# Optimization experiments

Hardware: AMD Instinct MI355X
Metric: run time of the kernel (lower is better)

## Reference

```python
import jax, jax.numpy as jnp
import numpy as np

B, S, D, H = 32, 512, 512, 8
DH = D // H
EXP_FF, EXP_CONV, K = 4, 2, 31
EPS = 1e-5


def _layernorm(x, g, b):
    m = jnp.mean(x, axis=-1, keepdims=True)
    v = jnp.mean(jnp.square(x - m), axis=-1, keepdims=True)
    return (x - m) * jax.lax.rsqrt(v + EPS) * g + b


def _sinusoid_pe(s, d):
    pos = np.arange(s, dtype=np.float32)[:, None]
    i = np.arange(0, d, 2, dtype=np.float32)[None, :]
    ang = pos / np.power(10000.0, i / d)
    pe = np.zeros((s, d), dtype=np.float32)
    pe[:, 0::2] = np.sin(ang)
    pe[:, 1::2] = np.cos(ang)
    return jnp.asarray(pe)


def _rel_shift(ps):
    # Transformer-XL relative shift on [b,h,s,s]
    b, h, s1, s2 = ps.shape
    p = jnp.pad(ps, ((0, 0), (0, 0), (0, 0), (1, 0)))
    p = p.reshape(b, h, s2 + 1, s1)
    return p[:, :, 1:].reshape(b, h, s1, s2)


def setup_inputs() -> dict:
    key = jax.random.key(0)
    ks = iter(jax.random.split(key, 64))
    nrm = lambda shape, sc=0.02: jax.random.normal(next(ks), shape, jnp.float32) * sc
    ones = lambda n: jnp.ones((n,), jnp.float32)
    zeros = lambda n: jnp.zeros((n,), jnp.float32)
    return {
        'x': jax.random.normal(next(ks), (B, S, D), jnp.float32),
        'ff1_g': ones(D), 'ff1_b': zeros(D),
        'ff1_w1': nrm((D, EXP_FF * D)), 'ff1_b1': zeros(EXP_FF * D),
        'ff1_w2': nrm((EXP_FF * D, D)), 'ff1_b2': zeros(D),
        'attn_g': ones(D), 'attn_b': zeros(D),
        'wq': nrm((D, D)), 'bq': zeros(D),
        'wk': nrm((D, D)), 'bk': zeros(D),
        'wv': nrm((D, D)), 'bv': zeros(D),
        'wpos': nrm((D, D)),
        'u_bias': nrm((H, DH)), 'v_bias': nrm((H, DH)),
        'wo': nrm((D, D)), 'bo': zeros(D),
        'conv_g': ones(D), 'conv_b': zeros(D),
        'pw1_w': nrm((D, EXP_CONV * D)), 'pw1_b': zeros(EXP_CONV * D),
        'dw_w': nrm((D, 1, K)),
        'bn_g': ones(D), 'bn_b': zeros(D), 'bn_m': zeros(D), 'bn_v': ones(D),
        'pw2_w': nrm((D, D)), 'pw2_b': zeros(D),
        'ff2_g': ones(D), 'ff2_b': zeros(D),
        'ff2_w1': nrm((D, EXP_FF * D)), 'ff2_b1': zeros(EXP_FF * D),
        'ff2_w2': nrm((EXP_FF * D, D)), 'ff2_b2': zeros(D),
        'ln_g': ones(D), 'ln_b': zeros(D),
    }


def _ff(x, g, b, w1, b1, w2, b2):
    y = _layernorm(x, g, b)
    return jnp.dot(jax.nn.silu(jnp.dot(y, w1) + b1), w2) + b2


def reference(x, ff1_g, ff1_b, ff1_w1, ff1_b1, ff1_w2, ff1_b2,
              attn_g, attn_b, wq, bq, wk, bk, wv, bv, wpos, u_bias, v_bias, wo, bo,
              conv_g, conv_b, pw1_w, pw1_b, dw_w, bn_g, bn_b, bn_m, bn_v, pw2_w, pw2_b,
              ff2_g, ff2_b, ff2_w1, ff2_b1, ff2_w2, ff2_b2, ln_g, ln_b):
    b, s, d = x.shape
    # Macaron FF 1 (half-step residual)
    out = x + 0.5 * _ff(x, ff1_g, ff1_b, ff1_w1, ff1_b1, ff1_w2, ff1_b2)
    # Relative-position multi-head self-attention
    y = _layernorm(out, attn_g, attn_b)
    pe = _sinusoid_pe(s, d)
    q = (jnp.dot(y, wq) + bq).reshape(b, s, H, DH)
    k = (jnp.dot(y, wk) + bk).reshape(b, s, H, DH)
    v = (jnp.dot(y, wv) + bv).reshape(b, s, H, DH)
    p = jnp.dot(pe, wpos).reshape(s, H, DH)
    content = jnp.einsum('bqhd,bkhd->bhqk', q + u_bias, k)
    pos = _rel_shift(jnp.einsum('bqhd,khd->bhqk', q + v_bias, p))
    attn = jax.nn.softmax((content + pos) / np.sqrt(d).astype(np.float32), axis=-1)
    ctx = jnp.einsum('bhqk,bkhd->bqhd', attn, v).reshape(b, s, d)
    out = out + (jnp.dot(ctx, wo) + bo)
    y = _layernorm(out, conv_g, conv_b)
    y = jnp.dot(y, pw1_w) + pw1_b                     # [b,s,2d]
    a, gate = jnp.split(y, 2, axis=-1)
    y = (a * jax.nn.sigmoid(gate)).transpose(0, 2, 1)  # [b,d,s]
    pad = (K - 1) // 2
    y = jax.lax.conv_general_dilated(y, dw_w, (1,), [(pad, pad)],
                                     dimension_numbers=('NCH', 'OIH', 'NCH'),
                                     feature_group_count=d)
    y = (y - bn_m[None, :, None]) * jax.lax.rsqrt(bn_v + EPS)[None, :, None] \
        * bn_g[None, :, None] + bn_b[None, :, None]
    y = jax.nn.silu(y).transpose(0, 2, 1)             # [b,s,d]
    out = out + (jnp.dot(y, pw2_w) + pw2_b)
    # Macaron FF 2 + final LN
    out = out + 0.5 * _ff(out, ff2_g, ff2_b, ff2_w1, ff2_b1, ff2_w2, ff2_b2)
    out = _layernorm(out, ln_g, ln_b)
    return out, attn
```

## Files before the change

### kernel.cpp

```cpp
#include <hip/hip_runtime.h>
#include <cstddef>
#include <cstdint>

#define EPSF 1e-5f

constexpr int BB = 32, SS = 512, DD = 512, HH = 8, DH = 64;
constexpr int NTOK = BB * SS;
constexpr size_t ND = (size_t)NTOK * DD;

typedef __attribute__((ext_vector_type(8))) short bf16x8;
typedef __attribute__((ext_vector_type(4))) float f32x4;

__device__ __forceinline__ float sigmf(float v) { return 1.f / (1.f + __expf(-v)); }

__device__ __forceinline__ ushort f2bf(float f) {
  union { float f; uint32_t u; } x{f};
  uint32_t r = x.u + 0x7FFF + ((x.u >> 16) & 1);
  return (ushort)(r >> 16);
}
__device__ __forceinline__ float bf2f(ushort u) {
  union { uint32_t u; float f; } x{(uint32_t)u << 16};
  return x.f;
}

__device__ __forceinline__ void gload16(const ushort* g, ushort* ldsbase) {
  __builtin_amdgcn_global_load_lds((const __attribute__((address_space(1))) void*)g,
                                   (__attribute__((address_space(3))) void*)ldsbase, 16, 0, 0);
}

__device__ __forceinline__ void xcd_swz(int& bx, int& by) {
  const int gx = gridDim.x;
  const int nwg = gx * gridDim.y;
  const int cpx = nwg >> 3;
  int id = by * gx + bx;
  id = (id & 7) * cpx + (id >> 3);
  bx = id % gx;
  by = id / gx;
}

__global__ __launch_bounds__(256) void ln_f32(const float* __restrict__ x,
                                              const float* __restrict__ g,
                                              const float* __restrict__ b,
                                              float* __restrict__ y) {
  const int lane = threadIdx.x & 63;
  const int row = blockIdx.x * 4 + (threadIdx.x >> 6);
  const float* xr = x + (size_t)row * 512;
  const float4 v0 = *(const float4*)&xr[lane << 2];
  const float4 v1 = *(const float4*)&xr[256 + (lane << 2)];
  float s = v0.x + v0.y + v0.z + v0.w + v1.x + v1.y + v1.z + v1.w;
#pragma unroll
  for (int o = 32; o > 0; o >>= 1) s += __shfl_xor(s, o);
  const float mean = s * (1.f / 512.f);
  float q = 0.f;
  q += (v0.x - mean) * (v0.x - mean); q += (v0.y - mean) * (v0.y - mean);
  q += (v0.z - mean) * (v0.z - mean); q += (v0.w - mean) * (v0.w - mean);
  q += (v1.x - mean) * (v1.x - mean); q += (v1.y - mean) * (v1.y - mean);
  q += (v1.z - mean) * (v1.z - mean); q += (v1.w - mean) * (v1.w - mean);
#pragma unroll
  for (int o = 32; o > 0; o >>= 1) q += __shfl_xor(q, o);
  const float rs = rsqrtf(q * (1.f / 512.f) + EPSF);
  const float4 g0 = *(const float4*)&g[lane << 2];
  const float4 g1 = *(const float4*)&g[256 + (lane << 2)];
  const float4 b0 = *(const float4*)&b[lane << 2];
  const float4 b1 = *(const float4*)&b[256 + (lane << 2)];
  float* yr = y + (size_t)row * 512;
  float4 o0, o1;
  o0.x = (v0.x - mean) * rs * g0.x + b0.x; o0.y = (v0.y - mean) * rs * g0.y + b0.y;
  o0.z = (v0.z - mean) * rs * g0.z + b0.z; o0.w = (v0.w - mean) * rs * g0.w + b0.w;
  o1.x = (v1.x - mean) * rs * g1.x + b1.x; o1.y = (v1.y - mean) * rs * g1.y + b1.y;
  o1.z = (v1.z - mean) * rs * g1.z + b1.z; o1.w = (v1.w - mean) * rs * g1.w + b1.w;
  *(float4*)&yr[lane << 2] = o0;
  *(float4*)&yr[256 + (lane << 2)] = o1;
}

__global__ __launch_bounds__(256) void ln_bf16(const float* __restrict__ x,
                                               const float* __restrict__ g,
                                               const float* __restrict__ b,
                                               ushort* __restrict__ y) {
  const int lane = threadIdx.x & 63;
  const int row = blockIdx.x * 4 + (threadIdx.x >> 6);
  const float* xr = x + (size_t)row * 512;
  const float4 v0 = *(const float4*)&xr[lane << 2];
  const float4 v1 = *(const float4*)&xr[256 + (lane << 2)];
  float s = v0.x + v0.y + v0.z + v0.w + v1.x + v1.y + v1.z + v1.w;
#pragma unroll
  for (int o = 32; o > 0; o >>= 1) s += __shfl_xor(s, o);
  const float mean = s * (1.f / 512.f);
  float q = 0.f;
  q += (v0.x - mean) * (v0.x - mean); q += (v0.y - mean) * (v0.y - mean);
  q += (v0.z - mean) * (v0.z - mean); q += (v0.w - mean) * (v0.w - mean);
  q += (v1.x - mean) * (v1.x - mean); q += (v1.y - mean) * (v1.y - mean);
  q += (v1.z - mean) * (v1.z - mean); q += (v1.w - mean) * (v1.w - mean);
#pragma unroll
  for (int o = 32; o > 0; o >>= 1) q += __shfl_xor(q, o);
  const float rs = rsqrtf(q * (1.f / 512.f) + EPSF);
  const float4 g0 = *(const float4*)&g[lane << 2];
  const float4 g1 = *(const float4*)&g[256 + (lane << 2)];
  const float4 b0 = *(const float4*)&b[lane << 2];
  const float4 b1 = *(const float4*)&b[256 + (lane << 2)];
  ushort* yr = y + (size_t)row * 512;
  ushort4 o0, o1;
  o0.x = f2bf((v0.x - mean) * rs * g0.x + b0.x); o0.y = f2bf((v0.y - mean) * rs * g0.y + b0.y);
  o0.z = f2bf((v0.z - mean) * rs * g0.z + b0.z); o0.w = f2bf((v0.w - mean) * rs * g0.w + b0.w);
  o1.x = f2bf((v1.x - mean) * rs * g1.x + b1.x); o1.y = f2bf((v1.y - mean) * rs * g1.y + b1.y);
  o1.z = f2bf((v1.z - mean) * rs * g1.z + b1.z); o1.w = f2bf((v1.w - mean) * rs * g1.w + b1.w);
  *(ushort4*)&yr[lane << 2] = o0;
  *(ushort4*)&yr[256 + (lane << 2)] = o1;
}

struct TpArgs {
  const float* src[11];
  ushort* dst[11];
  int K[11];
  int N[11];
  int base[12];
};

__global__ __launch_bounds__(256) void transpose_all(TpArgs a) {
  __shared__ float tile[32][33];
  int s = 0;
  const int bid = blockIdx.x;
  while (s < 10 && bid >= a.base[s + 1]) ++s;
  const int r = bid - a.base[s];
  const int K = a.K[s], N = a.N[s];
  const int ntx = N >> 5;
  const int n0 = (r % ntx) << 5;
  const int k0 = (r / ntx) << 5;
  const float* in = a.src[s];
  ushort* out = a.dst[s];
  const int tx = threadIdx.x & 31, ty = threadIdx.x >> 5;
#pragma unroll
  for (int i = 0; i < 32; i += 8)
    tile[ty + i][tx] = in[(size_t)(k0 + ty + i) * N + n0 + tx];
  __syncthreads();
#pragma unroll
  for (int i = 0; i < 32; i += 8)
    out[(size_t)(n0 + ty + i) * K + k0 + tx] = f2bf(tile[tx][ty + i]);
}

template <int ACT, int RES, int HB, int OBF>
__global__ __launch_bounds__(256) void gemm_bf16(const ushort* __restrict__ A,
                                                 const ushort* __restrict__ Wt,
                                                 const float* __restrict__ bias,
                                                 const float* __restrict__ res,
                                                 void* __restrict__ Cv,
                                                 int M, int K, int N) {
  __shared__ ushort Al[2][8192];
  __shared__ ushort Bl[2][8192];
  const int t = threadIdx.x;
  const int lane = t & 63;
  const int w = t >> 6;
  const int wr = (w >> 1) << 6, wc = (w & 1) << 6;
  int bx = blockIdx.x, by = blockIdx.y;
  xcd_swz(bx, by);
  const int m0 = by << 7, n0 = bx << 7;
  const int lm = lane & 15;
  const int grow = lane >> 3;
  const int gcol = (lane & 7) << 3;

  f32x4 acc[4][4];
#pragma unroll
  for (int i = 0; i < 4; ++i)
#pragma unroll
    for (int j = 0; j < 4; ++j) acc[i][j] = (f32x4)(0.f);

  const int NT = K >> 6;
#pragma unroll
  for (int i = 0; i < 4; ++i) {
    const int s = (w << 2) + i;
    gload16(A + (size_t)(m0 + (s << 3) + grow) * K + gcol, &Al[0][s << 9]);
    gload16(Wt + (size_t)(n0 + (s << 3) + grow) * K + gcol, &Bl[0][s << 9]);
  }
  __syncthreads();
  int cur = 0;
  for (int tt = 0; tt < NT; ++tt) {
    if (tt + 1 < NT) {
      const int k0 = (tt + 1) << 6;
#pragma unroll
      for (int i = 0; i < 4; ++i) {
        const int s = (w << 2) + i;
        gload16(A + (size_t)(m0 + (s << 3) + grow) * K + k0 + gcol, &Al[cur ^ 1][s << 9]);
        gload16(Wt + (size_t)(n0 + (s << 3) + grow) * K + k0 + gcol, &Bl[cur ^ 1][s << 9]);
      }
    }
#pragma unroll
    for (int ks = 0; ks < 2; ++ks) {
      const int kof = (ks << 5) + ((lane >> 4) << 3);
      bf16x8 af[4], bfr[4];
#pragma unroll
      for (int i = 0; i < 4; ++i) af[i] = *(const bf16x8*)&Al[cur][(wr + (i << 4) + lm) * 64 + kof];
#pragma unroll
      for (int j = 0; j < 4; ++j) bfr[j] = *(const bf16x8*)&Bl[cur][(wc + (j << 4) + lm) * 64 + kof];
#pragma unroll
      for (int i = 0; i < 4; ++i)
#pragma unroll
        for (int j = 0; j < 4; ++j)
          acc[i][j] = __builtin_amdgcn_mfma_f32_16x16x32_bf16(af[i], bfr[j], acc[i][j], 0, 0, 0);
    }
    __syncthreads();
    cur ^= 1;
  }

  float bb[4] = {0.f, 0.f, 0.f, 0.f};
  if (HB) {
#pragma unroll
    for (int j = 0; j < 4; ++j) bb[j] = bias[n0 + wc + j * 16 + lm];
  }
  const int rbase = m0 + wr + ((lane >> 4) << 2);
#pragma unroll
  for (int i = 0; i < 4; ++i) {
#pragma unroll
    for (int r = 0; r < 4; ++r) {
      const size_t row = (size_t)(rbase + i * 16 + r);
#pragma unroll
      for (int j = 0; j < 4; ++j) {
        const int col = n0 + wc + j * 16 + lm;
        float v = acc[i][j][r] + bb[j];
        if (ACT == 1) v = v * sigmf(v);
        if (RES == 1) v += res[row * N + col];
        else if (RES == 2) v = res[row * N + col] + 0.5f * v;
        if (OBF) ((ushort*)Cv)[row * N + col] = f2bf(v);
        else ((float*)Cv)[row * N + col] = v;
      }
    }
  }
}

__global__ __launch_bounds__(256) void gemm_qkv(const ushort* __restrict__ A,
                                                const ushort* __restrict__ Wt,
                                                const float* __restrict__ bq,
                                                const float* __restrict__ bk,
                                                const float* __restrict__ bv,
                                                const float* __restrict__ ub,
                                                const float* __restrict__ vb,
                                                ushort* __restrict__ qu,
                                                ushort* __restrict__ qv,
                                                ushort* __restrict__ kbb,
                                                ushort* __restrict__ vT,
                                                int M, int K) {
  __shared__ ushort Al[2][8192];
  __shared__ ushort Bl[2][8192];
  const int t = threadIdx.x;
  const int lane = t & 63;
  const int w = t >> 6;
  const int wr = (w >> 1) << 6, wc = (w & 1) << 6;
  int bx = blockIdx.x, by = blockIdx.y;
  xcd_swz(bx, by);
  const int m0 = by << 7, n0 = bx << 7;
  const int lm = lane & 15;
  const int grow = lane >> 3;
  const int gcol = (lane & 7) << 3;
  f32x4 acc[4][4];
#pragma unroll
  for (int i = 0; i < 4; ++i)
#pragma unroll
    for (int j = 0; j < 4; ++j) acc[i][j] = (f32x4)(0.f);
  const int NT = K >> 6;
#pragma unroll
  for (int i = 0; i < 4; ++i) {
    const int s = (w << 2) + i;
    gload16(A + (size_t)(m0 + (s << 3) + grow) * K + gcol, &Al[0][s << 9]);
    gload16(Wt + (size_t)(n0 + (s << 3) + grow) * K + gcol, &Bl[0][s << 9]);
  }
  __syncthreads();
  int cur = 0;
  for (int tt = 0; tt < NT; ++tt) {
    if (tt + 1 < NT) {
      const int k0 = (tt + 1) << 6;
#pragma unroll
      for (int i = 0; i < 4; ++i) {
        const int s = (w << 2) + i;
        gload16(A + (size_t)(m0 + (s << 3) + grow) * K + k0 + gcol, &Al[cur ^ 1][s << 9]);
        gload16(Wt + (size_t)(n0 + (s << 3) + grow) * K + k0 + gcol, &Bl[cur ^ 1][s << 9]);
      }
    }
#pragma unroll
    for (int ks = 0; ks < 2; ++ks) {
      const int kof = (ks << 5) + ((lane >> 4) << 3);
      bf16x8 af[4], bfr[4];
#pragma unroll
      for (int i = 0; i < 4; ++i) af[i] = *(const bf16x8*)&Al[cur][(wr + (i << 4) + lm) * 64 + kof];
#pragma unroll
      for (int j = 0; j < 4; ++j) bfr[j] = *(const bf16x8*)&Bl[cur][(wc + (j << 4) + lm) * 64 + kof];
#pragma unroll
      for (int i = 0; i < 4; ++i)
#pragma unroll
        for (int j = 0; j < 4; ++j)
          acc[i][j] = __builtin_amdgcn_mfma_f32_16x16x32_bf16(af[i], bfr[j], acc[i][j], 0, 0, 0);
    }
    __syncthreads();
    cur ^= 1;
  }
  const int seg = n0 >> 9;
  const int nloc = n0 & 511;
  const float* bsel = (seg == 0) ? bq : (seg == 1 ? bk : bv);
  float bb[4], uu[4], vv[4];
#pragma unroll
  for (int j = 0; j < 4; ++j) {
    const int col = nloc + wc + j * 16 + lm;
    bb[j] = bsel[col];
    if (seg == 0) { uu[j] = ub[col]; vv[j] = vb[col]; }
  }
  const int rbase = m0 + wr + ((lane >> 4) << 2);
  if (seg == 2) {
    const int bloc = m0 >> 9;
    const int sbase = rbase - (bloc << 9);
#pragma unroll
    for (int i = 0; i < 4; ++i) {
#pragma unroll
      for (int j = 0; j < 4; ++j) {
        const int col = nloc + wc + j * 16 + lm;
        ushort4 o;
        o.x = f2bf(acc[i][j][0] + bb[j]);
        o.y = f2bf(acc[i][j][1] + bb[j]);
        o.z = f2bf(acc[i][j][2] + bb[j]);
        o.w = f2bf(acc[i][j][3] + bb[j]);
        *(ushort4*)&vT[((size_t)((bloc << 9) + col)) * 512 + sbase + i * 16] = o;
      }
    }
    return;
  }
#pragma unroll
  for (int i = 0; i < 4; ++i) {
#pragma unroll
    for (int r = 0; r < 4; ++r) {
      const size_t row = (size_t)(rbase + i * 16 + r);
#pragma unroll
      for (int j = 0; j < 4; ++j) {
        const int col = nloc + wc + j * 16 + lm;
        const float v = acc[i][j][r] + bb[j];
        if (seg == 0) {
          qu[row * 512 + col] = f2bf(v + uu[j]);
          qv[row * 512 + col] = f2bf(v + vv[j]);
        } else {
          kbb[row * 512 + col] = f2bf(v);
        }
      }
    }
  }
}

__global__ __launch_bounds__(256) void gemm_glu(const ushort* __restrict__ A,
                                                const ushort* __restrict__ Wt,
                                                const float* __restrict__ bias,
                                                ushort* __restrict__ Cout,
                                                int M, int K) {
  __shared__ ushort Al[8192];
  __shared__ ushort Ba[8192];
  __shared__ ushort Bg[8192];
  const int t = threadIdx.x;
  const int lane = t & 63;
  const int w = t >> 6;
  const int wr = (w >> 1) << 6, wc = (w & 1) << 6;
  int bx = blockIdx.x, by = blockIdx.y;
  xcd_swz(bx, by);
  const int m0 = by << 7, n0 = bx << 7;
  const int lm = lane & 15;
  const int grow = lane >> 3;
  const int gcol = (lane & 7) << 3;
  const ushort* WtA = Wt;
  const ushort* WtG = Wt + (size_t)512 * 512;
  f32x4 acca[4][4], accg[4][4];
#pragma unroll
  for (int i = 0; i < 4; ++i)
#pragma unroll
    for (int j = 0; j < 4; ++j) { acca[i][j] = (f32x4)(0.f); accg[i][j] = (f32x4)(0.f); }
  const int NT = K >> 6;
  for (int tt = 0; tt < NT; ++tt) {
    const int k0 = tt << 6;
    if (tt) __syncthreads();
#pragma unroll
    for (int i = 0; i < 4; ++i) {
      const int s = (w << 2) + i;
      gload16(A + (size_t)(m0 + (s << 3) + grow) * K + k0 + gcol, &Al[s << 9]);
      gload16(WtA + (size_t)(n0 + (s << 3) + grow) * K + k0 + gcol, &Ba[s << 9]);
      gload16(WtG + (size_t)(n0 + (s << 3) + grow) * K + k0 + gcol, &Bg[s << 9]);
    }
    __syncthreads();
#pragma unroll
    for (int ks = 0; ks < 2; ++ks) {
      const int kof = (ks << 5) + ((lane >> 4) << 3);
      bf16x8 af[4], ba4[4], bg4[4];
#pragma unroll
      for (int i = 0; i < 4; ++i) af[i] = *(const bf16x8*)&Al[(wr + (i << 4) + lm) * 64 + kof];
#pragma unroll
      for (int j = 0; j < 4; ++j) {
        ba4[j] = *(const bf16x8*)&Ba[(wc + (j << 4) + lm) * 64 + kof];
        bg4[j] = *(const bf16x8*)&Bg[(wc + (j << 4) + lm) * 64 + kof];
      }
#pragma unroll
      for (int i = 0; i < 4; ++i)
#pragma unroll
        for (int j = 0; j < 4; ++j) {
          acca[i][j] = __builtin_amdgcn_mfma_f32_16x16x32_bf16(af[i], ba4[j], acca[i][j], 0, 0, 0);
          accg[i][j] = __builtin_amdgcn_mfma_f32_16x16x32_bf16(af[i], bg4[j], accg[i][j], 0, 0, 0);
        }
    }
  }
  float bba[4], bbg[4];
#pragma unroll
  for (int j = 0; j < 4; ++j) {
    const int col = n0 + wc + j * 16 + lm;
    bba[j] = bias[col];
    bbg[j] = bias[512 + col];
  }
  const int rbase = m0 + wr + ((lane >> 4) << 2);
#pragma unroll
  for (int i = 0; i < 4; ++i) {
#pragma unroll
    for (int r = 0; r < 4; ++r) {
      const size_t row = (size_t)(rbase + i * 16 + r);
#pragma unroll
      for (int j = 0; j < 4; ++j) {
        const int col = n0 + wc + j * 16 + lm;
        const float va = acca[i][j][r] + bba[j];
        const float vg = accg[i][j][r] + bbg[j];
        Cout[row * 512 + col] = f2bf(va * sigmf(vg));
      }
    }
  }
}

__global__ void pe_kernel_bf16(ushort* __restrict__ pe) {
  const int pos = blockIdx.x, ii = threadIdx.x;
  const float ang = (float)pos * powf(10000.f, -(float)(2 * ii) / 512.f);
  pe[((size_t)pos << 9) + 2 * ii] = f2bf(sinf(ang));
  pe[((size_t)pos << 9) + 2 * ii + 1] = f2bf(cosf(ang));
}

__global__ __launch_bounds__(256) void attn_fused3(const ushort* __restrict__ qu,
                                                   const ushort* __restrict__ qv,
                                                   const ushort* __restrict__ kbb,
                                                   const ushort* __restrict__ ppb,
                                                   const ushort* __restrict__ vT,
                                                   float* __restrict__ attn,
                                                   ushort* __restrict__ ctx) {
  __shared__ ushort psL[65][520];
  __shared__ ushort stage[64][72];
  const int t = threadIdx.x, lane = t & 63, w = t >> 6;
  const int z = blockIdx.y, b = z >> 3, h = z & 7;
  const int q0 = blockIdx.x << 6;
  const int lm = lane & 15, lk = (lane >> 4) << 3;
  const int fr4 = (lane >> 4) << 2;
  const int srow = t >> 2, scol = (t & 3) << 4;

  const size_t qoff = ((size_t)((b << 9) + q0 + (w << 4) + lm)) * 512 + (h << 6);
  bf16x8 a0 = *(const bf16x8*)&qv[qoff + lk];
  bf16x8 a1 = *(const bf16x8*)&qv[qoff + lk + 32];
  int er = q0 + 64 + lm;
  if (er > 511) er = 511;
  const size_t eoff = ((size_t)((b << 9) + er)) * 512 + (h << 6);
  const bf16x8 e0 = *(const bf16x8*)&qv[eoff + lk];
  const bf16x8 e1 = *(const bf16x8*)&qv[eoff + lk + 32];
  const ushort* pb_ = ppb + (h << 6);
#pragma unroll
  for (int tile = 0; tile < 8; ++tile) {
    __syncthreads();
    {
      const ushort* src = &pb_[(size_t)((tile << 6) + srow) * 512 + scol];
      *(bf16x8*)&stage[srow][scol] = *(const bf16x8*)src;
      *(bf16x8*)&stage[srow][scol + 8] = *(const bf16x8*)(src + 8);
    }
    __syncthreads();
#pragma unroll
    for (int ctl = 0; ctl < 4; ++ctl) {
      const bf16x8 b0 = *(const bf16x8*)&stage[(ctl << 4) + lm][lk];
      const bf16x8 b1 = *(const bf16x8*)&stage[(ctl << 4) + lm][lk + 32];
      f32x4 a = (f32x4)(0.f);
      a = __builtin_amdgcn_mfma_f32_16x16x32_bf16(a0, b0, a, 0, 0, 0);
      a = __builtin_amdgcn_mfma_f32_16x16x32_bf16(a1, b1, a, 0, 0, 0);
      const int col = (tile << 6) + (ctl << 4) + lm;
#pragma unroll
      for (int r = 0; r < 4; ++r) psL[(w << 4) + fr4 + r][col] = f2bf(a[r]);
    }
    {
      const bf16x8 b0 = *(const bf16x8*)&stage[(w << 4) + lm][lk];
      const bf16x8 b1 = *(const bf16x8*)&stage[(w << 4) + lm][lk + 32];
      f32x4 a = (f32x4)(0.f);
      a = __builtin_amdgcn_mfma_f32_16x16x32_bf16(e0, b0, a, 0, 0, 0);
      a = __builtin_amdgcn_mfma_f32_16x16x32_bf16(e1, b1, a, 0, 0, 0);
      if ((lane >> 4) == 0) psL[64][(tile << 6) + (w << 4) + lm] = f2bf(a[0]);
    }
  }

  a0 = *(const bf16x8*)&qu[qoff + lk];
  a1 = *(const bf16x8*)&qu[qoff + lk + 32];
  const ushort* kb_ = kbb + ((size_t)(b << 9)) * 512 + (h << 6);
  f32x4 acc[32];
#pragma unroll
  for (int i = 0; i < 32; ++i) acc[i] = (f32x4)(0.f);
#pragma unroll
  for (int tile = 0; tile < 8; ++tile) {
    __syncthreads();
    {
      const ushort* src = &kb_[(size_t)((tile << 6) + srow) * 512 + scol];
      *(bf16x8*)&stage[srow][scol] = *(const bf16x8*)src;
      *(bf16x8*)&stage[srow][scol + 8] = *(const bf16x8*)(src + 8);
    }
    __syncthreads();
#pragma unroll
    for (int ctl = 0; ctl < 4; ++ctl) {
      const int ct = (tile << 2) + ctl;
      const bf16x8 b0 = *(const bf16x8*)&stage[(ctl << 4) + lm][lk];
      const bf16x8 b1 = *(const bf16x8*)&stage[(ctl << 4) + lm][lk + 32];
      acc[ct] = __builtin_amdgcn_mfma_f32_16x16x32_bf16(a0, b0, acc[ct], 0, 0, 0);
      acc[ct] = __builtin_amdgcn_mfma_f32_16x16x32_bf16(a1, b1, acc[ct], 0, 0, 0);
    }
  }

  const float scale = 0.044194173824159216f;
  const int qb_ = q0 + (w << 4) + fr4;
#pragma unroll
  for (int ct = 0; ct < 32; ++ct) {
#pragma unroll
    for (int r = 0; r < 4; ++r) {
      const int q = qb_ + r;
      const int qq = q - q0;
      const int c = (ct << 4) + lm;
      float f;
      if (c <= q)          f = bf2f(psL[qq][c - q + 511]);
      else if (c == q + 1) f = 0.f;
      else                 f = bf2f(psL[qq + 1][c - q - 2]);
      acc[ct][r] = (acc[ct][r] + f) * scale;
    }
  }
  float mx[4] = {-3.0e38f, -3.0e38f, -3.0e38f, -3.0e38f};
#pragma unroll
  for (int ct = 0; ct < 32; ++ct)
#pragma unroll
    for (int r = 0; r < 4; ++r) mx[r] = fmaxf(mx[r], acc[ct][r]);
#pragma unroll
  for (int o = 1; o < 16; o <<= 1)
#pragma unroll
    for (int r = 0; r < 4; ++r) mx[r] = fmaxf(mx[r], __shfl_xor(mx[r], o));
  float sme[4] = {0.f, 0.f, 0.f, 0.f};
#pragma unroll
  for (int ct = 0; ct < 32; ++ct)
#pragma unroll
    for (int r = 0; r < 4; ++r) {
      acc[ct][r] = __expf(acc[ct][r] - mx[r]);
      sme[r] += acc[ct][r];
    }
#pragma unroll
  for (int o = 1; o < 16; o <<= 1)
#pragma unroll
    for (int r = 0; r < 4; ++r) sme[r] += __shfl_xor(sme[r], o);
#pragma unroll
  for (int r = 0; r < 4; ++r) {
    const float inv = 1.f / sme[r];
#pragma unroll
    for (int ct = 0; ct < 32; ++ct) acc[ct][r] *= inv;
  }
  float* arow = attn + ((size_t)((b << 3) + h) << 18);
#pragma unroll
  for (int ct = 0; ct < 32; ++ct)
#pragma unroll
    for (int r = 0; r < 4; ++r)
      arow[(size_t)(qb_ + r) * 512 + (ct << 4) + lm] = acc[ct][r];
  ushort* Pl = &psL[0][0];
  f32x4 acc2[4];
#pragma unroll
  for (int i = 0; i < 4; ++i) acc2[i] = (f32x4)(0.f);
  const ushort* vtb = vT + ((size_t)((b << 9) + (h << 6))) * 512;
#pragma unroll
  for (int ch = 0; ch < 8; ++ch) {
    __syncthreads();
#pragma unroll
    for (int ctl = 0; ctl < 4; ++ctl) {
      const int ct = (ch << 2) + ctl;
#pragma unroll
      for (int r = 0; r < 4; ++r)
        Pl[((w << 4) + fr4 + r) * 72 + (ctl << 4) + lm] = f2bf(acc[ct][r]);
    }
    {
      const ushort* src = &vtb[(size_t)srow * 512 + (ch << 6) + scol];
      *(bf16x8*)&stage[srow][scol] = *(const bf16x8*)src;
      *(bf16x8*)&stage[srow][scol + 8] = *(const bf16x8*)(src + 8);
    }
    __syncthreads();
#pragma unroll
    for (int ks = 0; ks < 2; ++ks) {
      const int kof = (ks << 5) + lk;
      const bf16x8 pbf = *(const bf16x8*)&Pl[((w << 4) + lm) * 72 + kof];
#pragma unroll
      for (int dt = 0; dt < 4; ++dt) {
        const bf16x8 va = *(const bf16x8*)&stage[(dt << 4) + lm][kof];
        acc2[dt] = __builtin_amdgcn_mfma_f32_16x16x32_bf16(va, pbf, acc2[dt], 0, 0, 0);
      }
    }
  }
  const int qq2 = q0 + (w << 4) + lm;
  const int dbase = fr4;
#pragma unroll
  for (int dt = 0; dt < 4; ++dt) {
    ushort4 o;
    o.x = f2bf(acc2[dt][0]); o.y = f2bf(acc2[dt][1]);
    o.z = f2bf(acc2[dt][2]); o.w = f2bf(acc2[dt][3]);
    *(ushort4*)&ctx[((size_t)((b << 9) + qq2)) * 512 + (h << 6) + (dt << 4) + dbase] = o;
  }
}

__global__ __launch_bounds__(256) void dwconv2(const ushort* __restrict__ in,
                                               const float* __restrict__ w,
                                               const float* __restrict__ bng,
                                               const float* __restrict__ bnb,
                                               const float* __restrict__ bnm,
                                               const float* __restrict__ bnv,
                                               ushort* __restrict__ out) {
  __shared__ float wl[31][128];
  const int t = threadIdx.x;
  const int dbase = blockIdx.x << 7;
  const int b = blockIdx.z;
  const int sb = (blockIdx.y << 6) + ((t >> 6) << 4);
  if (t < 128) {
    const float* ws = &w[(dbase + t) * 31];
#pragma unroll
    for (int k = 0; k < 31; ++k) wl[k][t] = ws[k];
  }
  __syncthreads();
  const int dl = (t & 63) << 1;
  const int d = dbase + dl;
  const size_t base = (((size_t)b) << 18) + d;
  float2 win[46];
#pragma unroll
  for (int i = 0; i < 46; ++i) {
    const int s = sb - 15 + i;
    if (s >= 0 && s < 512) {
      const ushort2 u = *(const ushort2*)&in[base + ((size_t)s << 9)];
      win[i].x = bf2f(u.x); win[i].y = bf2f(u.y);
    } else {
      win[i].x = 0.f; win[i].y = 0.f;
    }
  }
  float2 acc[16];
#pragma unroll
  for (int p = 0; p < 16; ++p) { acc[p].x = 0.f; acc[p].y = 0.f; }
#pragma unroll
  for (int k = 0; k < 31; ++k) {
    const float2 w2 = *(const float2*)&wl[k][dl];
#pragma unroll
    for (int p = 0; p < 16; ++p) {
      acc[p].x = fmaf(win[p + k].x, w2.x, acc[p].x);
      acc[p].y = fmaf(win[p + k].y, w2.y, acc[p].y);
    }
  }
  const float g0 = bng[d] * rsqrtf(bnv[d] + EPSF);
  const float g1 = bng[d + 1] * rsqrtf(bnv[d + 1] + EPSF);
  const float m0 = bnm[d], m1 = bnm[d + 1];
  const float bb0 = bnb[d], bb1 = bnb[d + 1];
#pragma unroll
  for (int p = 0; p < 16; ++p) {
    float v0 = (acc[p].x - m0) * g0 + bb0;
    float v1 = (acc[p].y - m1) * g1 + bb1;
    v0 = v0 * sigmf(v0);
    v1 = v1 * sigmf(v1);
    ushort2 o;
    o.x = f2bf(v0); o.y = f2bf(v1);
    *(ushort2*)&out[base + ((size_t)(sb + p) << 9)] = o;
  }
}

extern "C" void kernel_launch(void* const* d_in, const int* in_sizes, int n_in,
                              void* d_out, int out_size, void* d_ws, size_t ws_size,
                              hipStream_t stream) {
  const float* x      = (const float*)d_in[0];
  const float* ff1_g  = (const float*)d_in[1];
  const float* ff1_b  = (const float*)d_in[2];
  const float* ff1_w1 = (const float*)d_in[3];
  const float* ff1_b1 = (const float*)d_in[4];
  const float* ff1_w2 = (const float*)d_in[5];
  const float* ff1_b2 = (const float*)d_in[6];
  const float* attn_g = (const float*)d_in[7];
  const float* attn_b = (const float*)d_in[8];
  const float* wq     = (const float*)d_in[9];
  const float* bq     = (const float*)d_in[10];
  const float* wk     = (const float*)d_in[11];
  const float* bk     = (const float*)d_in[12];
  const float* wv     = (const float*)d_in[13];
  const float* bv     = (const float*)d_in[14];
  const float* wpos   = (const float*)d_in[15];
  const float* u_bias = (const float*)d_in[16];
  const float* v_bias = (const float*)d_in[17];
  const float* wo     = (const float*)d_in[18];
  const float* bo     = (const float*)d_in[19];
  const float* conv_g = (const float*)d_in[20];
  const float* conv_b = (const float*)d_in[21];
  const float* pw1_w  = (const float*)d_in[22];
  const float* pw1_b  = (const float*)d_in[23];
  const float* dw_w   = (const float*)d_in[24];
  const float* bn_g   = (const float*)d_in[25];
  const float* bn_b   = (const float*)d_in[26];
  const float* bn_m   = (const float*)d_in[27];
  const float* bn_v   = (const float*)d_in[28];
  const float* pw2_w  = (const float*)d_in[29];
  const float* pw2_b  = (const float*)d_in[30];
  const float* ff2_g  = (const float*)d_in[31];
  const float* ff2_b  = (const float*)d_in[32];
  const float* ff2_w1 = (const float*)d_in[33];
  const float* ff2_b1 = (const float*)d_in[34];
  const float* ff2_w2 = (const float*)d_in[35];
  const float* ff2_b2 = (const float*)d_in[36];
  const float* ln_g   = (const float*)d_in[37];
  const float* ln_b   = (const float*)d_in[38];

  float* out  = (float*)d_out;
  float* attn = out + ND;

  float*  res  = (float*)d_ws;
  ushort* ybf  = (ushort*)(res + ND);
  float*  big  = (float*)(ybf + ND);
  ushort* vT   = (ushort*)(big + 2 * ND);
  ushort* dwbf = vT + ND;
  ushort* wts  = dwbf + ND;
  ushort* pebf = wts + 6291456;
  ushort* ppbf = pebf + 262144;

  ushort* ffmid = (ushort*)big;
  ushort* qu    = (ushort*)big;
  ushort* qv    = qu + ND;
  ushort* kbb   = qv + ND;
  ushort* ctxbf = ybf;
  ushort* glubf = (ushort*)big;

  ushort* ff1w1t = wts;
  ushort* ff1w2t = wts + 1048576;
  ushort* wqt    = wts + 2097152;
  ushort* wkt    = wts + 2359296;
  ushort* wvt    = wts + 2621440;
  ushort* wot    = wts + 2883584;
  ushort* pw1t   = wts + 3145728;
  ushort* pw2t   = wts + 3670016;
  ushort* ff2w1t = wts + 3932160;
  ushort* ff2w2t = wts + 4980736;
  ushort* wpost  = wts + 6029312;

  const dim3 blk(256);

  TpArgs ta;
  auto set = [&](int i, const float* s, ushort* d, int K, int N) {
    ta.src[i] = s; ta.dst[i] = d; ta.K[i] = K; ta.N[i] = N;
  };
  set(0, ff1_w1, ff1w1t, 512, 2048);
  set(1, ff1_w2, ff1w2t, 2048, 512);
  set(2, wq, wqt, 512, 512);
  set(3, wk, wkt, 512, 512);
  set(4, wv, wvt, 512, 512);
  set(5, wo, wot, 512, 512);
  set(6, wpos, wpost, 512, 512);
  set(7, pw1_w, pw1t, 512, 1024);
  set(8, pw2_w, pw2t, 512, 512);
  set(9, ff2_w1, ff2w1t, 512, 2048);
  set(10, ff2_w2, ff2w2t, 2048, 512);
  int tacc = 0;
  for (int i = 0; i < 11; ++i) { ta.base[i] = tacc; tacc += (ta.N[i] >> 5) * (ta.K[i] >> 5); }
  ta.base[11] = tacc;
  transpose_all<<<tacc, blk, 0, stream>>>(ta);
  pe_kernel_bf16<<<512, blk, 0, stream>>>(pebf);
  gemm_bf16<0, 0, 0, 1><<<dim3(4, 4), blk, 0, stream>>>(pebf, wpost, nullptr, nullptr, ppbf,
                                                        512, 512, 512);

  ln_bf16<<<NTOK / 4, blk, 0, stream>>>(x, ff1_g, ff1_b, ybf);
  gemm_bf16<1, 0, 1, 1><<<dim3(16, 128), blk, 0, stream>>>(ybf, ff1w1t, ff1_b1, nullptr, ffmid,
                                                           NTOK, 512, 2048);
  gemm_bf16<0, 2, 1, 0><<<dim3(4, 128), blk, 0, stream>>>(ffmid, ff1w2t, ff1_b2, x, res,
                                                          NTOK, 2048, 512);

  ln_bf16<<<NTOK / 4, blk, 0, stream>>>(res, attn_g, attn_b, ybf);
  gemm_qkv<<<dim3(12, 128), blk, 0, stream>>>(ybf, wqt, bq, bk, bv, u_bias, v_bias,
                                              qu, qv, kbb, vT, NTOK, 512);
  attn_fused3<<<dim3(8, 256), blk, 0, stream>>>(qu, qv, kbb, ppbf, vT, attn, ctxbf);
  gemm_bf16<0, 1, 1, 0><<<dim3(4, 128), blk, 0, stream>>>(ctxbf, wot, bo, res, res,
                                                          NTOK, 512, 512);

  ln_bf16<<<NTOK / 4, blk, 0, stream>>>(res, conv_g, conv_b, ybf);
  gemm_glu<<<dim3(4, 128), blk, 0, stream>>>(ybf, pw1t, pw1_b, glubf, NTOK, 512);
  dwconv2<<<dim3(4, 8, 32), blk, 0, stream>>>(glubf, dw_w, bn_g, bn_b, bn_m, bn_v, dwbf);
  gemm_bf16<0, 1, 1, 0><<<dim3(4, 128), blk, 0, stream>>>(dwbf, pw2t, pw2_b, res, res,
                                                          NTOK, 512, 512);

  ln_bf16<<<NTOK / 4, blk, 0, stream>>>(res, ff2_g, ff2_b, ybf);
  gemm_bf16<1, 0, 1, 1><<<dim3(16, 128), blk, 0, stream>>>(ybf, ff2w1t, ff2_b1, nullptr, ffmid,
                                                           NTOK, 512, 2048);
  gemm_bf16<0, 2, 1, 0><<<dim3(4, 128), blk, 0, stream>>>(ffmid, ff2w2t, ff2_b2, res, res,
                                                          NTOK, 2048, 512);
  ln_f32<<<NTOK / 4, blk, 0, stream>>>(res, ln_g, ln_b, out);
}
```

Before: 823.1 us.

## Load attention MFMA B-operands directly from global, drop LDS staging and syncs

The attention kernel no longer stages positional, key and value tiles through a shared-memory buffer. Each wave reads its MFMA B fragments straight from global memory (through L1/L2), which removes the staging buffer and most of the block-wide barriers. The extra-row positional product is spread across waves by tile index. This cuts LDS traffic and barrier stalls, but each wave now issues redundant, strided global loads of the same K/V/P rows, which depends on cache hit rates.

```diff
diff --git a/kernel.cpp b/kernel.cpp
--- a/kernel.cpp
+++ b/kernel.cpp
@@ -428,7 +428,7 @@
   pe[((size_t)pos << 9) + 2 * ii + 1] = f2bf(cosf(ang));
 }
 
-__global__ __launch_bounds__(256) void attn_fused3(const ushort* __restrict__ qu,
+__global__ __launch_bounds__(256) void attn_fused4(const ushort* __restrict__ qu,
                                                    const ushort* __restrict__ qv,
                                                    const ushort* __restrict__ kbb,
                                                    const ushort* __restrict__ ppb,
@@ -436,77 +436,55 @@
                                                    float* __restrict__ attn,
                                                    ushort* __restrict__ ctx) {
   __shared__ ushort psL[65][520];
-  __shared__ ushort stage[64][72];
   const int t = threadIdx.x, lane = t & 63, w = t >> 6;
   const int z = blockIdx.y, b = z >> 3, h = z & 7;
   const int q0 = blockIdx.x << 6;
-  const int lm = lane & 15, lk = (lane >> 4) << 3;
-  const int fr4 = (lane >> 4) << 2;
-  const int srow = t >> 2, scol = (t & 3) << 4;
+  const int lm = lane & 15, g = lane >> 4;
+  const int lk = g << 3, fr4 = g << 2;
 
   const size_t qoff = ((size_t)((b << 9) + q0 + (w << 4) + lm)) * 512 + (h << 6);
-  bf16x8 a0 = *(const bf16x8*)&qv[qoff + lk];
-  bf16x8 a1 = *(const bf16x8*)&qv[qoff + lk + 32];
+  const bf16x8 av0 = *(const bf16x8*)&qv[qoff + lk];
+  const bf16x8 av1 = *(const bf16x8*)&qv[qoff + lk + 32];
+  const bf16x8 au0 = *(const bf16x8*)&qu[qoff + lk];
+  const bf16x8 au1 = *(const bf16x8*)&qu[qoff + lk + 32];
   int er = q0 + 64 + lm;
   if (er > 511) er = 511;
   const size_t eoff = ((size_t)((b << 9) + er)) * 512 + (h << 6);
   const bf16x8 e0 = *(const bf16x8*)&qv[eoff + lk];
   const bf16x8 e1 = *(const bf16x8*)&qv[eoff + lk + 32];
+
   const ushort* pb_ = ppb + (h << 6);
 #pragma unroll
-  for (int tile = 0; tile < 8; ++tile) {
-    __syncthreads();
-    {
-      const ushort* src = &pb_[(size_t)((tile << 6) + srow) * 512 + scol];
-      *(bf16x8*)&stage[srow][scol] = *(const bf16x8*)src;
-      *(bf16x8*)&stage[srow][scol + 8] = *(const bf16x8*)(src + 8);
-    }
-    __syncthreads();
-#pragma unroll
-    for (int ctl = 0; ctl < 4; ++ctl) {
-      const bf16x8 b0 = *(const bf16x8*)&stage[(ctl << 4) + lm][lk];
-      const bf16x8 b1 = *(const bf16x8*)&stage[(ctl << 4) + lm][lk + 32];
-      f32x4 a = (f32x4)(0.f);
-      a = __builtin_amdgcn_mfma_f32_16x16x32_bf16(a0, b0, a, 0, 0, 0);
-      a = __builtin_amdgcn_mfma_f32_16x16x32_bf16(a1, b1, a, 0, 0, 0);
-      const int col = (tile << 6) + (ctl << 4) + lm;
-#pragma unroll
-      for (int r = 0; r < 4; ++r) psL[(w << 4) + fr4 + r][col] = f2bf(a[r]);
-    }
-    {
-      const bf16x8 b0 = *(const bf16x8*)&stage[(w << 4) + lm][lk];
-      const bf16x8 b1 = *(const bf16x8*)&stage[(w << 4) + lm][lk + 32];
-      f32x4 a = (f32x4)(0.f);
-      a = __builtin_amdgcn_mfma_f32_16x16x32_bf16(e0, b0, a, 0, 0, 0);
-      a = __builtin_amdgcn_mfma_f32_16x16x32_bf16(e1, b1, a, 0, 0, 0);
-      if ((lane >> 4) == 0) psL[64][(tile << 6) + (w << 4) + lm] = f2bf(a[0]);
-    }
-  }
-
-  a0 = *(const bf16x8*)&qu[qoff + lk];
-  a1 = *(const bf16x8*)&qu[qoff + lk + 32];
+  for (int jt = 0; jt < 32; ++jt) {
+    const ushort* pr = pb_ + (size_t)((jt << 4) + lm) * 512;
+    const bf16x8 b0 = *(const bf16x8*)&pr[lk];
+    const bf16x8 b1 = *(const bf16x8*)&pr[lk + 32];
+    f32x4 a = (f32x4)(0.f);
+    a = __builtin_amdgcn_mfma_f32_16x16x32_bf16(av0, b0, a, 0, 0, 0);
+    a = __builtin_amdgcn_mfma_f32_16x16x32_bf16(av1, b1, a, 0, 0, 0);
+#pragma unroll
+    for (int r = 0; r < 4; ++r) psL[(w << 4) + fr4 + r][(jt << 4) + lm] = f2bf(a[r]);
+    if ((jt & 3) == w) {
+      f32x4 e = (f32x4)(0.f);
+      e = __builtin_amdgcn_mfma_f32_16x16x32_bf16(e0, b0, e, 0, 0, 0);
+      e = __builtin_amdgcn_mfma_f32_16x16x32_bf16(e1, b1, e, 0, 0, 0);
+      if (g == 0) psL[64][(jt << 4) + lm] = f2bf(e[0]);
+    }
+  }
+
+  f32x4 acc[32];
+#pragma unroll
+  for (int i = 0; i < 32; ++i) acc[i] = (f32x4)(0.f);
   const ushort* kb_ = kbb + ((size_t)(b << 9)) * 512 + (h << 6);
-  f32x4 acc[32];
-#pragma unroll
-  for (int i = 0; i < 32; ++i) acc[i] = (f32x4)(0.f);
-#pragma unroll
-  for (int tile = 0; tile < 8; ++tile) {
-    __syncthreads();
-    {
-      const ushort* src = &kb_[(size_t)((tile << 6) + srow) * 512 + scol];
-      *(bf16x8*)&stage[srow][scol] = *(const bf16x8*)src;
-      *(bf16x8*)&stage[srow][scol + 8] = *(const bf16x8*)(src + 8);
-    }
-    __syncthreads();
-#pragma unroll
-    for (int ctl = 0; ctl < 4; ++ctl) {
-      const int ct = (tile << 2) + ctl;
-      const bf16x8 b0 = *(const bf16x8*)&stage[(ctl << 4) + lm][lk];
-      const bf16x8 b1 = *(const bf16x8*)&stage[(ctl << 4) + lm][lk + 32];
-      acc[ct] = __builtin_amdgcn_mfma_f32_16x16x32_bf16(a0, b0, acc[ct], 0, 0, 0);
-      acc[ct] = __builtin_amdgcn_mfma_f32_16x16x32_bf16(a1, b1, acc[ct], 0, 0, 0);
-    }
-  }
+#pragma unroll
+  for (int ct = 0; ct < 32; ++ct) {
+    const ushort* kr = kb_ + (size_t)((ct << 4) + lm) * 512;
+    const bf16x8 b0 = *(const bf16x8*)&kr[lk];
+    const bf16x8 b1 = *(const bf16x8*)&kr[lk + 32];
+    acc[ct] = __builtin_amdgcn_mfma_f32_16x16x32_bf16(au0, b0, acc[ct], 0, 0, 0);
+    acc[ct] = __builtin_amdgcn_mfma_f32_16x16x32_bf16(au1, b1, acc[ct], 0, 0, 0);
+  }
+  __syncthreads();
 
   const float scale = 0.044194173824159216f;
   const int qb_ = q0 + (w << 4) + fr4;
@@ -557,6 +535,8 @@
 #pragma unroll
     for (int r = 0; r < 4; ++r)
       arow[(size_t)(qb_ + r) * 512 + (ct << 4) + lm] = acc[ct][r];
+  __syncthreads();
+
   ushort* Pl = &psL[0][0];
   f32x4 acc2[4];
 #pragma unroll
@@ -564,7 +544,6 @@
   const ushort* vtb = vT + ((size_t)((b << 9) + (h << 6))) * 512;
 #pragma unroll
   for (int ch = 0; ch < 8; ++ch) {
-    __syncthreads();
 #pragma unroll
     for (int ctl = 0; ctl < 4; ++ctl) {
       const int ct = (ch << 2) + ctl;
@@ -572,31 +551,25 @@
       for (int r = 0; r < 4; ++r)
         Pl[((w << 4) + fr4 + r) * 72 + (ctl << 4) + lm] = f2bf(acc[ct][r]);
     }
-    {
-      const ushort* src = &vtb[(size_t)srow * 512 + (ch << 6) + scol];
-      *(bf16x8*)&stage[srow][scol] = *(const bf16x8*)src;
-      *(bf16x8*)&stage[srow][scol + 8] = *(const bf16x8*)(src + 8);
-    }
-    __syncthreads();
 #pragma unroll
     for (int ks = 0; ks < 2; ++ks) {
       const int kof = (ks << 5) + lk;
       const bf16x8 pbf = *(const bf16x8*)&Pl[((w << 4) + lm) * 72 + kof];
 #pragma unroll
       for (int dt = 0; dt < 4; ++dt) {
-        const bf16x8 va = *(const bf16x8*)&stage[(dt << 4) + lm][kof];
+        const bf16x8 va =
+            *(const bf16x8*)&vtb[(size_t)((dt << 4) + lm) * 512 + (ch << 6) + kof];
         acc2[dt] = __builtin_amdgcn_mfma_f32_16x16x32_bf16(va, pbf, acc2[dt], 0, 0, 0);
       }
     }
   }
   const int qq2 = q0 + (w << 4) + lm;
-  const int dbase = fr4;
 #pragma unroll
   for (int dt = 0; dt < 4; ++dt) {
     ushort4 o;
     o.x = f2bf(acc2[dt][0]); o.y = f2bf(acc2[dt][1]);
     o.z = f2bf(acc2[dt][2]); o.w = f2bf(acc2[dt][3]);
-    *(ushort4*)&ctx[((size_t)((b << 9) + qq2)) * 512 + (h << 6) + (dt << 4) + dbase] = o;
+    *(ushort4*)&ctx[((size_t)((b << 9) + qq2)) * 512 + (h << 6) + (dt << 4) + fr4] = o;
   }
 }
 
@@ -768,7 +741,7 @@
   ln_bf16<<<NTOK / 4, blk, 0, stream>>>(res, attn_g, attn_b, ybf);
   gemm_qkv<<<dim3(12, 128), blk, 0, stream>>>(ybf, wqt, bq, bk, bv, u_bias, v_bias,
                                               qu, qv, kbb, vT, NTOK, 512);
-  attn_fused3<<<dim3(8, 256), blk, 0, stream>>>(qu, qv, kbb, ppbf, vT, attn, ctxbf);
+  attn_fused4<<<dim3(8, 256), blk, 0, stream>>>(qu, qv, kbb, ppbf, vT, attn, ctxbf);
   gemm_bf16<0, 1, 1, 0><<<dim3(4, 128), blk, 0, stream>>>(ctxbf, wot, bo, res, res,
                                                           NTOK, 512, 512);
 
```

Measured after the change: 961.0 us. +16.8%, slower.
